# Optimization experiments

Measured on AMD Instinct MI355X. Metric: run time of the kernel, lower is better.

## Reference

```python
import jax, jax.numpy as jnp
import numpy as np

B, T, D, H = 4, 1024, 1024, 16
TP = 1024
HD = D // H
LN_EPS = 1e-3  # keras LayerNormalization default epsilon


def snac_linear(x, wt, mt):
    # conv1dsnac: w = tanh(wt) * sigmoid(mt), shape [1, nx, nf] -> [nx, nf]
    w = (jnp.tanh(wt) * jax.nn.sigmoid(mt))[0]
    return jnp.einsum('btx,xf->btf', x, w)


def layernorm(x, gamma, beta):
    mu = jnp.mean(x, axis=-1, keepdims=True)
    var = jnp.mean(jnp.square(x - mu), axis=-1, keepdims=True)
    return (x - mu) * jax.lax.rsqrt(var + LN_EPS) * gamma + beta


def setup_inputs() -> dict:
    key = jax.random.key(0)
    ks = jax.random.split(key, 10)
    s = 0.02
    return {
        'input': jax.random.normal(ks[0], (B, T, D), jnp.float32),
        'past': jax.random.normal(ks[1], (B, 2, H, TP, HD), jnp.float32),
        'qkv_wt': jax.random.normal(ks[2], (1, D, 3 * D), jnp.float32) * s,
        'qkv_mt': jax.random.normal(ks[3], (1, D, 3 * D), jnp.float32) * s,
        'merge_wt': jax.random.normal(ks[4], (1, D, D), jnp.float32) * s,
        'merge_mt': jax.random.normal(ks[5], (1, D, D), jnp.float32) * s,
        'ln1_wt': jax.random.normal(ks[6], (1, D, D), jnp.float32) * s,
        'ln1_mt': jax.random.normal(ks[7], (1, D, D), jnp.float32) * s,
        'g1': jnp.ones((D,), jnp.float32), 'b1': jnp.zeros((D,), jnp.float32),
        'g2': jnp.ones((D,), jnp.float32), 'b2': jnp.zeros((D,), jnp.float32),
    }


def reference(input, past, qkv_wt, qkv_mt, merge_wt, merge_mt, ln1_wt, ln1_mt, g1, b1, g2, b2):
    x = input
    xn = layernorm(x, g1, b1)
    c = snac_linear(xn, qkv_wt, qkv_mt)  # [B, T, 3D]
    q, k, v = jnp.split(c, 3, axis=2)
    # split heads -> [B, H, T, HD]
    to_heads = lambda t: t.reshape(B, T, H, HD).transpose(0, 2, 1, 3)
    q, k, v = to_heads(q), to_heads(k), to_heads(v)
    present = jnp.stack([k, v], axis=1)  # [B, 2, H, T, HD]
    pk, pv = past[:, 0], past[:, 1]
    k = jnp.concatenate([pk, k], axis=2)  # [B, H, TP+T, HD]
    v = jnp.concatenate([pv, v], axis=2)
    nd, ns = T, TP + T
    w = jnp.einsum('bhqd,bhkd->bhqk', q, k) * jax.lax.rsqrt(jnp.float32(HD))
    i = jnp.arange(nd)[:, None]
    j = jnp.arange(ns)[None, :]
    m = (i >= j - ns + nd).astype(w.dtype)  # [nd, ns] causal mask incl. past
    w = w * m - jnp.asarray(1e10, w.dtype) * (1 - m)
    msk = jax.nn.softmax(w, axis=-1)  # [B, H, T, TP+T]
    a = jnp.einsum('bhqk,bhkd->bhqd', msk, v)
    ah = a.transpose(0, 2, 1, 3).reshape(B, T, D)  # merge heads
    am = snac_linear(ah, merge_wt, merge_mt)
    xa = x + am
    mlp = snac_linear(layernorm(xa, g2, b2), ln1_wt, ln1_mt)
    xm = xa + mlp
    return xm, present, msk
```

## Files before the change

kernel.cpp:

```cpp
#include <hip/hip_runtime.h>
#include <hip/hip_bf16.h>

typedef _Float16 half8 __attribute__((ext_vector_type(8)));
typedef _Float16 half4v __attribute__((ext_vector_type(4)));
typedef float f32x4 __attribute__((ext_vector_type(4)));

#define DEV static __device__ __forceinline__


typedef __attribute__((address_space(1))) const unsigned int* gas_p;
typedef __attribute__((address_space(3))) unsigned int* las_p;
DEV void glds16(const void* g, void* s) {
  __builtin_amdgcn_global_load_lds((gas_p)g, (las_p)s, 16, 0, 0);
}

__global__ __launch_bounds__(256) void prep_all(const float* __restrict__ qkv_wt,
                                                const float* __restrict__ qkv_mt,
                                                const float* __restrict__ mg_wt,
                                                const float* __restrict__ mg_mt,
                                                const float* __restrict__ l1_wt,
                                                const float* __restrict__ l1_mt,
                                                _Float16* __restrict__ wq,
                                                _Float16* __restrict__ wm,
                                                _Float16* __restrict__ wl) {
  __shared__ float tile[64][65];
  const float *wt, *mt;
  _Float16* out;
  int N, bid;
  if (blockIdx.x < 768) {
    wt = qkv_wt; mt = qkv_mt; out = wq; N = 3072; bid = blockIdx.x;
  } else if (blockIdx.x < 1024) {
    wt = mg_wt; mt = mg_mt; out = wm; N = 1024; bid = blockIdx.x - 768;
  } else {
    wt = l1_wt; mt = l1_mt; out = wl; N = 1024; bid = blockIdx.x - 1024;
  }
  const int ntiles = N >> 6;
  const int nt = bid % ntiles, kt = bid / ntiles;
  const int k0 = kt << 6, n0 = nt << 6;
  const int t = threadIdx.x, r = t >> 2, c0 = (t & 3) << 4;
  const long ibase = (long)(k0 + r) * N + n0 + c0;
#pragma unroll
  for (int j = 0; j < 16; j += 4) {
    float4 a = *(const float4*)(wt + ibase + j);
    float4 b = *(const float4*)(mt + ibase + j);
    tile[r][c0 + j + 0] = tanhf(a.x) / (1.f + __expf(-b.x));
    tile[r][c0 + j + 1] = tanhf(a.y) / (1.f + __expf(-b.y));
    tile[r][c0 + j + 2] = tanhf(a.z) / (1.f + __expf(-b.z));
    tile[r][c0 + j + 3] = tanhf(a.w) / (1.f + __expf(-b.w));
  }
  __syncthreads();
  half8 o0, o1;
#pragma unroll
  for (int j = 0; j < 8; ++j) {
    o0[j] = (_Float16)tile[c0 + j][r];
    o1[j] = (_Float16)tile[c0 + 8 + j][r];
  }
  _Float16* dst = out + (long)(n0 + r) * 1024 + k0 + c0;
  *(half8*)dst = o0;
  *(half8*)(dst + 8) = o1;
}

__global__ __launch_bounds__(256) void kv_prep(const float* __restrict__ past,
                                               const _Float16* __restrict__ vnew,
                                               _Float16* __restrict__ kf,
                                               _Float16* __restrict__ vt) {
  __shared__ float tile[64][65];
  if (blockIdx.x < 4096) {
    const long e = ((long)blockIdx.x * 256 + threadIdx.x) * 4;
    const int b = (int)(e >> 20);
    const int rem = (int)(e & 1048575);
    float4 v = *(const float4*)(past + (long)b * 2097152 + rem);
    half4v o = {(_Float16)v.x, (_Float16)v.y, (_Float16)v.z, (_Float16)v.w};
    const int h = rem >> 16, td = rem & 65535;
    *(half4v*)(kf + (long)(b * 16 + h) * 131072 + td) = o;
    return;
  }
  const int bid = blockIdx.x - 4096;
  const int bh = bid >> 5, kt = bid & 31;
  const int b = bh >> 4, h = bh & 15;
  const int k0 = kt << 6;
  const int t = threadIdx.x, r = t >> 2, c0 = (t & 3) << 4;
  if (k0 < 1024) {
    const float* src = past + (((long)(b * 2 + 1) * 16 + h) * 1024 + (k0 + r)) * 64 + c0;
#pragma unroll
    for (int j = 0; j < 16; j += 4) {
      float4 v = *(const float4*)(src + j);
      tile[r][c0 + j + 0] = v.x;
      tile[r][c0 + j + 1] = v.y;
      tile[r][c0 + j + 2] = v.z;
      tile[r][c0 + j + 3] = v.w;
    }
  } else {
    const _Float16* src = vnew + ((long)bh * 1024 + (k0 - 1024 + r)) * 64 + c0;
    half8 a = *(const half8*)src;
    half8 bq = *(const half8*)(src + 8);
#pragma unroll
    for (int j = 0; j < 8; ++j) {
      tile[r][c0 + j] = (float)a[j];
      tile[r][c0 + 8 + j] = (float)bq[j];
    }
  }
  __syncthreads();
  half8 o0, o1;
#pragma unroll
  for (int j = 0; j < 8; ++j) {
    o0[j] = (_Float16)tile[c0 + j][r];
    o1[j] = (_Float16)tile[c0 + 8 + j][r];
  }
  _Float16* dst = vt + ((long)bh * 64 + r) * 2048 + k0 + c0;
  *(half8*)dst = o0;
  *(half8*)(dst + 8) = o1;
}

template <int F16IN>
__global__ __launch_bounds__(256) void ln_k(const void* __restrict__ xin,
                                            const float* __restrict__ g,
                                            const float* __restrict__ be,
                                            _Float16* __restrict__ out) {
  __shared__ float red[4];
  const int row = blockIdx.x, tid = threadIdx.x, l = tid & 63, w = tid >> 6;
  float v0, v1, v2, v3;
  if constexpr (F16IN == 0) {
    float4 v = *(const float4*)((const float*)xin + (long)row * 1024 + tid * 4);
    v0 = v.x; v1 = v.y; v2 = v.z; v3 = v.w;
  } else {
    half4v v = *(const half4v*)((const _Float16*)xin + (long)row * 1024 + tid * 4);
    v0 = (float)v[0]; v1 = (float)v[1]; v2 = (float)v[2]; v3 = (float)v[3];
  }
  float s = v0 + v1 + v2 + v3;
#pragma unroll
  for (int o = 32; o > 0; o >>= 1) s += __shfl_down(s, o, 64);
  if (l == 0) red[w] = s;
  __syncthreads();
  const float mu = (red[0] + red[1] + red[2] + red[3]) * (1.f / 1024.f);
  float dx = v0 - mu, dy = v1 - mu, dz = v2 - mu, dw = v3 - mu;
  float ss = dx * dx + dy * dy + dz * dz + dw * dw;
#pragma unroll
  for (int o = 32; o > 0; o >>= 1) ss += __shfl_down(ss, o, 64);
  __syncthreads();
  if (l == 0) red[w] = ss;
  __syncthreads();
  const float var = (red[0] + red[1] + red[2] + red[3]) * (1.f / 1024.f);
  const float rs = rsqrtf(var + 1e-3f);
  float4 gv = *(const float4*)(g + tid * 4);
  float4 bv = *(const float4*)(be + tid * 4);
  half4v o = {(_Float16)(dx * rs * gv.x + bv.x), (_Float16)(dy * rs * gv.y + bv.y),
              (_Float16)(dz * rs * gv.z + bv.z), (_Float16)(dw * rs * gv.w + bv.w)};
  *(half4v*)(out + (long)row * 1024 + tid * 4) = o;
}

template <int BM, int EPI>
__global__ __launch_bounds__(256) void gemm_k(const _Float16* __restrict__ A,
                                              const _Float16* __restrict__ Bt,
                                              int mtiles,
                                              _Float16* __restrict__ e_q,
                                              _Float16* __restrict__ e_k,
                                              _Float16* __restrict__ e_v,
                                              float* __restrict__ e_present,
                                              const void* __restrict__ e_resv,
                                              void* __restrict__ e_outv) {
  constexpr int FM = BM / 32;
  __shared__ __align__(16) char smem[2 * BM * 128 + 32768];
  char* Bbase = smem + 2 * BM * 128;
  const int tid = threadIdx.x, l = tid & 63, w = tid >> 6;
  const int wm = w >> 1, wn = w & 1;
  const int bm = blockIdx.x % mtiles, bn = blockIdx.x / mtiles;
  const long m0 = (long)bm * BM, n0 = (long)bn * 128;

  f32x4 acc[FM][4];
#pragma unroll
  for (int i = 0; i < FM; ++i)
#pragma unroll
    for (int j = 0; j < 4; ++j) acc[i][j] = (f32x4){0.f, 0.f, 0.f, 0.f};

  auto stage = [&](int b, int kt) {
#pragma unroll
    for (int i = 0; i < FM; ++i) {
      const int cid = i * 256 + tid, row = cid >> 3, u = cid & 7;
      glds16(A + (m0 + row) * 1024 + kt * 64 + ((u ^ (row & 7)) << 3),
             smem + b * BM * 128 + i * 4096 + w * 1024);
    }
#pragma unroll
    for (int i = 0; i < 4; ++i) {
      const int cid = i * 256 + tid, row = cid >> 3, u = cid & 7;
      glds16(Bt + (n0 + row) * 1024 + kt * 64 + ((u ^ (row & 7)) << 3),
             Bbase + b * 16384 + i * 4096 + w * 1024);
    }
  };

  stage(0, 0);
  __syncthreads();
  for (int kt = 0; kt < 16; ++kt) {
    const int cur = kt & 1;
    if (kt < 15) stage(cur ^ 1, kt + 1);
    const char* As = smem + cur * BM * 128;
    const char* Bs = Bbase + cur * 16384;
    __builtin_amdgcn_s_setprio(1);
#pragma unroll
    for (int k2 = 0; k2 < 2; ++k2) {
      const int sl = k2 * 4 + (l >> 4);
      half8 bfr[4];
#pragma unroll
      for (int fn = 0; fn < 4; ++fn) {
        const int rn = wn * 64 + fn * 16 + (l & 15);
        bfr[fn] = *(const half8*)(Bs + rn * 128 + ((sl ^ (rn & 7)) << 4));
      }
#pragma unroll
      for (int fm = 0; fm < FM; ++fm) {
        const int rm = wm * (BM / 2) + fm * 16 + (l & 15);
        const half8 afr = *(const half8*)(As + rm * 128 + ((sl ^ (rm & 7)) << 4));
#pragma unroll
        for (int fn = 0; fn < 4; ++fn)
          acc[fm][fn] = __builtin_amdgcn_mfma_f32_16x16x32_f16(afr, bfr[fn], acc[fm][fn], 0, 0, 0);
      }
    }
    __builtin_amdgcn_s_setprio(0);
    __syncthreads();
  }
#pragma unroll
  for (int fm = 0; fm < FM; ++fm) {
#pragma unroll
    for (int fn = 0; fn < 4; ++fn) {
#pragma unroll
      for (int r = 0; r < 4; ++r) {
        const long row = m0 + wm * (BM / 2) + fm * 16 + (l >> 4) * 4 + r;
        const long col = n0 + fn * 16 + (l & 15) + wn * 64;
        const float v = acc[fm][fn][r];
        if constexpr (EPI == 0) {
          const int b = (int)(row >> 10), t = (int)(row & 1023);
          const int sec = (int)(col >> 10), h = ((int)col >> 6) & 15, hd = (int)col & 63;
          const long bh = b * 16 + h;
          if (sec == 0) {
            e_q[(bh * 1024 + t) * 64 + hd] = (_Float16)v;
          } else if (sec == 1) {
            e_present[(((long)(b * 2) * 16 + h) * 1024 + t) * 64 + hd] = v;
            e_k[(bh * 2048 + 1024 + t) * 64 + hd] = (_Float16)v;
          } else {
            e_present[(((long)(b * 2 + 1) * 16 + h) * 1024 + t) * 64 + hd] = v;
            e_v[(bh * 1024 + t) * 64 + hd] = (_Float16)v;
          }
        } else if constexpr (EPI == 1) {
          ((_Float16*)e_outv)[row * 1024 + col] =
              (_Float16)(((const float*)e_resv)[row * 1024 + col] + v);
        } else {
          ((float*)e_outv)[row * 1024 + col] =
              (float)((const _Float16*)e_resv)[row * 1024 + col] + v;
        }
      }
    }
  }
}

__global__ __launch_bounds__(256, 4) void attn_k(const _Float16* __restrict__ qg,
                                                 const _Float16* __restrict__ kg,
                                                 const _Float16* __restrict__ vtg,
                                                 float* __restrict__ msk,
                                                 _Float16* __restrict__ ah) {
  __shared__ __align__(16) char smem[40960];
  char* ps_all = smem + 32768;
  const int tid = threadIdx.x, l = tid & 63, w = tid >> 6;
  char* psw = ps_all + w * 2048;
  const int lq = l & 15, hi = l >> 4;

  const int x = blockIdx.x & 7, g = blockIdx.x >> 3;
  const int bh = (g & 7) * 8 + x;
  const int qt = 15 - (g >> 3);
  const int r0 = qt << 6;
  const int rowg0 = r0 + w * 16;

  const _Float16* kb = kg + (long)bh * 131072;
  const _Float16* vb = vtg + (long)bh * 131072;
  float* mskb = msk + ((long)bh * 1024 + rowg0) * 2048;

  half8 qa[2];
  {
    const _Float16* qp = qg + ((long)bh * 1024 + rowg0 + lq) * 64 + hi * 8;
    qa[0] = *(const half8*)qp;
    qa[1] = *(const half8*)(qp + 32);
  }

  constexpr float C1 = 0.125f * 1.44269504088896341f;
  const int lim = rowg0 + lq + 1024;

  const int nc1 = (r0 + 1215) >> 7;
  auto stageK128 = [&](int b, int c) {
#pragma unroll
    for (int i = 0; i < 4; ++i) {
      const int cid = i * 256 + tid, row = cid >> 3, u = cid & 7;
      glds16(kb + (long)(c * 128 + row) * 64 + ((u ^ (row & 7)) << 3),
             smem + b * 16384 + i * 4096 + w * 1024);
    }
  };
  float rsum = 0.f;
  stageK128(0, 0);
  __syncthreads();
  for (int c = 0; c < nc1; ++c) {
    const int cur = c & 1;
    if (c + 1 < nc1) stageK128(cur ^ 1, c + 1);
    const char* ks = smem + cur * 16384;
    f32x4 sa[8];
#pragma unroll
    for (int fn = 0; fn < 8; ++fn) sa[fn] = (f32x4){0.f, 0.f, 0.f, 0.f};
    __builtin_amdgcn_s_setprio(1);
#pragma unroll
    for (int k2 = 0; k2 < 2; ++k2) {
      const int sl = k2 * 4 + hi;
      half8 ak[8];
#pragma unroll
      for (int fn = 0; fn < 8; ++fn) {
        const int rn = fn * 16 + lq;
        ak[fn] = *(const half8*)(ks + rn * 128 + ((sl ^ (rn & 7)) << 4));
      }
#pragma unroll
      for (int fn = 0; fn < 8; ++fn)
        sa[fn] = __builtin_amdgcn_mfma_f32_16x16x32_f16(ak[fn], qa[k2], sa[fn], 0, 0, 0);
    }
    __builtin_amdgcn_s_setprio(0);
    if (c < nc1 - 1) {
#pragma unroll
      for (int fn = 0; fn < 8; ++fn)
#pragma unroll
        for (int r = 0; r < 4; ++r) rsum += __builtin_amdgcn_exp2f(sa[fn][r] * C1);
    } else {
#pragma unroll
      for (int fn = 0; fn < 8; ++fn)
#pragma unroll
        for (int r = 0; r < 4; ++r) {
          const int col = c * 128 + fn * 16 + hi * 4 + r;
          const float e = __builtin_amdgcn_exp2f(sa[fn][r] * C1);
          rsum += (col <= lim) ? e : 0.f;
        }
    }
    __syncthreads();
  }
  rsum += __shfl_xor(rsum, 16, 64);
  rsum += __shfl_xor(rsum, 32, 64);
  const float c2s = -__builtin_amdgcn_logf(rsum);

  const int nc = (r0 + 1151) >> 6;
  auto stageK = [&](int b, int c) {
#pragma unroll
    for (int i = 0; i < 2; ++i) {
      const int cid = i * 256 + tid, row = cid >> 3, u = cid & 7;
      glds16(kb + (long)(c * 64 + row) * 64 + ((u ^ (row & 7)) << 3),
             smem + b * 8192 + i * 4096 + w * 1024);
    }
  };
  auto stageV = [&](int b, int c) {
#pragma unroll
    for (int i = 0; i < 2; ++i) {
      const int cid = i * 256 + tid, row = cid >> 3, u = cid & 7;
      glds16(vb + (long)row * 2048 + c * 64 + ((u ^ (row & 7)) << 3),
             smem + 16384 + b * 8192 + i * 4096 + w * 1024);
    }
  };

  f32x4 pv[4];
#pragma unroll
  for (int j = 0; j < 4; ++j) pv[j] = (f32x4){0.f, 0.f, 0.f, 0.f};
  __syncthreads();
  stageK(0, 0);
  stageV(0, 0);
  __syncthreads();
  for (int c = 0; c < nc; ++c) {
    const int cur = c & 1;
    if (c + 1 < nc) {
      stageK(cur ^ 1, c + 1);
      stageV(cur ^ 1, c + 1);
    }
    const char* ks = smem + cur * 8192;
    f32x4 sa[4];
#pragma unroll
    for (int fn = 0; fn < 4; ++fn) sa[fn] = (f32x4){0.f, 0.f, 0.f, 0.f};
    __builtin_amdgcn_s_setprio(1);
#pragma unroll
    for (int k2 = 0; k2 < 2; ++k2) {
      const int sl = k2 * 4 + hi;
      half8 ak[4];
#pragma unroll
      for (int fn = 0; fn < 4; ++fn) {
        const int rn = fn * 16 + lq;
        ak[fn] = *(const half8*)(ks + rn * 128 + ((sl ^ (rn & 7)) << 4));
      }
#pragma unroll
      for (int fn = 0; fn < 4; ++fn)
        sa[fn] = __builtin_amdgcn_mfma_f32_16x16x32_f16(ak[fn], qa[k2], sa[fn], 0, 0, 0);
    }
    __builtin_amdgcn_s_setprio(0);
    const bool bound = (c == nc - 1);
#pragma unroll
    for (int fn = 0; fn < 4; ++fn) {
      float pr[4];
#pragma unroll
      for (int r = 0; r < 4; ++r) {
        float p = __builtin_amdgcn_exp2f(sa[fn][r] * C1 + c2s);
        if (bound) {
          const int col = c * 64 + fn * 16 + hi * 4 + r;
          p = (col <= lim) ? p : 0.f;
        }
        pr[r] = p;
      }
      *(float4*)(mskb + (long)lq * 2048 + c * 64 + fn * 16 + hi * 4) =
          make_float4(pr[0], pr[1], pr[2], pr[3]);
      const half4v hv = {(_Float16)pr[0], (_Float16)pr[1], (_Float16)pr[2],
                         (_Float16)pr[3]};
      const int bc = fn * 32 + hi * 8;
      *(half4v*)(psw + lq * 128 + ((((bc >> 4) ^ (lq & 7)) << 4) | (bc & 15))) = hv;
    }
    __builtin_amdgcn_wave_barrier();
    asm volatile("s_waitcnt lgkmcnt(0)" ::: "memory");
    __builtin_amdgcn_sched_barrier(0);
    const char* vs = smem + 16384 + cur * 8192;
    __builtin_amdgcn_s_setprio(1);
#pragma unroll
    for (int k2p = 0; k2p < 2; ++k2p) {
      const int sl2 = k2p * 4 + hi;
      const half8 pa = *(const half8*)(psw + lq * 128 + ((sl2 ^ (lq & 7)) << 4));
      half8 bv[4];
#pragma unroll
      for (int fn2 = 0; fn2 < 4; ++fn2) {
        const int rd = fn2 * 16 + lq;
        bv[fn2] = *(const half8*)(vs + rd * 128 + ((sl2 ^ (rd & 7)) << 4));
      }
#pragma unroll
      for (int fn2 = 0; fn2 < 4; ++fn2)
        pv[fn2] = __builtin_amdgcn_mfma_f32_16x16x32_f16(pa, bv[fn2], pv[fn2], 0, 0, 0);
    }
    __builtin_amdgcn_s_setprio(0);
    __syncthreads();
  }

  const int ntail = 512 - (nc << 4);
  if (ntail > 0) {
    const float4 z4 = make_float4(0.f, 0.f, 0.f, 0.f);
    for (int row = 0; row < 16; ++row)
      for (int i = l; i < ntail; i += 64)
        *(float4*)(mskb + (long)row * 2048 + nc * 64 + i * 4) = z4;
  }

  const int b_ = bh >> 4, h_ = bh & 15;
  _Float16* ahb = ah + ((long)b_ * 1024 + rowg0) * 1024 + h_ * 64;
#pragma unroll
  for (int fn2 = 0; fn2 < 4; ++fn2)
#pragma unroll
    for (int r = 0; r < 4; ++r)
      ahb[(long)(hi * 4 + r) * 1024 + fn2 * 16 + lq] = (_Float16)pv[fn2][r];
}

extern "C" void kernel_launch(void* const* d_in, const int* in_sizes, int n_in,
                              void* d_out, int out_size, void* d_ws, size_t ws_size,
                              hipStream_t stream) {
  const float* x = (const float*)d_in[0];
  const float* past = (const float*)d_in[1];
  const float* qkv_wt = (const float*)d_in[2];
  const float* qkv_mt = (const float*)d_in[3];
  const float* merge_wt = (const float*)d_in[4];
  const float* merge_mt = (const float*)d_in[5];
  const float* ln1_wt = (const float*)d_in[6];
  const float* ln1_mt = (const float*)d_in[7];
  const float* g1 = (const float*)d_in[8];
  const float* b1 = (const float*)d_in[9];
  const float* g2 = (const float*)d_in[10];
  const float* b2 = (const float*)d_in[11];

  float* out = (float*)d_out;
  float* o_xm = out;
  float* o_present = out + 4194304;
  float* o_msk = out + 4194304 + 8388608;

  char* ws = (char*)d_ws;
  _Float16* wq_t = (_Float16*)(ws + 0);
  _Float16* wm_t = (_Float16*)(ws + 6291456);
  _Float16* wl_t = (_Float16*)(ws + 8388608);
  _Float16* xn   = (_Float16*)(ws + 10485760);
  _Float16* qws  = (_Float16*)(ws + 18874368);
  _Float16* kful = (_Float16*)(ws + 27262976);
  _Float16* vnew = (_Float16*)(ws + 44040192);
  _Float16* vt   = (_Float16*)(ws + 52428800);
  _Float16* ah   = (_Float16*)(ws + 69206016);
  _Float16* xa   = (_Float16*)(ws + 77594624);

  prep_all<<<1280, 256, 0, stream>>>(qkv_wt, qkv_mt, merge_wt, merge_mt, ln1_wt,
                                     ln1_mt, wq_t, wm_t, wl_t);
  ln_k<0><<<4096, 256, 0, stream>>>(x, g1, b1, xn);
  gemm_k<128, 0><<<768, 256, 0, stream>>>(xn, wq_t, 32, qws, kful, vnew, o_present,
                                          nullptr, nullptr);
  kv_prep<<<6144, 256, 0, stream>>>(past, vnew, kful, vt);
  attn_k<<<1024, 256, 0, stream>>>(qws, kful, vt, o_msk, ah);
  gemm_k<64, 1><<<512, 256, 0, stream>>>(ah, wm_t, 64, nullptr, nullptr, nullptr,
                                         nullptr, x, xa);
  ln_k<1><<<4096, 256, 0, stream>>>(xa, g2, b2, xn);
  gemm_k<64, 2><<<512, 256, 0, stream>>>(xn, wl_t, 64, nullptr, nullptr, nullptr,
                                         nullptr, xa, o_xm);
}
```

Baseline: 289.0 us.

## Drop GEMM LDS double buffering and use 64x64 tiles for merge/MLP GEMMs

The GEMM kernel now stages A and B into a single LDS buffer each k-step and waits on a barrier before computing, instead of prefetching the next k-tile into a second buffer. It also gains a BN template parameter so the merge and MLP projections can run 64x64 tiles over 1024 blocks instead of 64x128 over 512. The aim is to cut LDS use per block so more blocks fit per CU, and to spread the small GEMMs across more workgroups. The cost is that global-to-LDS loads no longer overlap MFMA work within a block, so the kernel must rely on other resident blocks to hide load latency. Each block also reuses less data with the smaller tiles.

```diff
diff --git a/kernel.cpp b/kernel.cpp
--- a/kernel.cpp
+++ b/kernel.cpp
@@ -149,7 +149,7 @@
   *(half4v*)(out + (long)row * 1024 + tid * 4) = o;
 }
 
-template <int BM, int EPI>
+template <int BM, int BN, int EPI>
 __global__ __launch_bounds__(256) void gemm_k(const _Float16* __restrict__ A,
                                               const _Float16* __restrict__ Bt,
                                               int mtiles,
@@ -159,50 +159,43 @@
                                               float* __restrict__ e_present,
                                               const void* __restrict__ e_resv,
                                               void* __restrict__ e_outv) {
-  constexpr int FM = BM / 32;
-  __shared__ __align__(16) char smem[2 * BM * 128 + 32768];
-  char* Bbase = smem + 2 * BM * 128;
+  constexpr int FM = BM / 32, FN = BN / 32;
+  __shared__ __align__(16) char smem[BM * 128 + BN * 128];
+  char* As = smem;
+  char* Bs = smem + BM * 128;
   const int tid = threadIdx.x, l = tid & 63, w = tid >> 6;
   const int wm = w >> 1, wn = w & 1;
   const int bm = blockIdx.x % mtiles, bn = blockIdx.x / mtiles;
-  const long m0 = (long)bm * BM, n0 = (long)bn * 128;
-
-  f32x4 acc[FM][4];
+  const long m0 = (long)bm * BM, n0 = (long)bn * BN;
+
+  f32x4 acc[FM][FN];
 #pragma unroll
   for (int i = 0; i < FM; ++i)
 #pragma unroll
-    for (int j = 0; j < 4; ++j) acc[i][j] = (f32x4){0.f, 0.f, 0.f, 0.f};
-
-  auto stage = [&](int b, int kt) {
+    for (int j = 0; j < FN; ++j) acc[i][j] = (f32x4){0.f, 0.f, 0.f, 0.f};
+
+  for (int kt = 0; kt < 16; ++kt) {
 #pragma unroll
     for (int i = 0; i < FM; ++i) {
       const int cid = i * 256 + tid, row = cid >> 3, u = cid & 7;
       glds16(A + (m0 + row) * 1024 + kt * 64 + ((u ^ (row & 7)) << 3),
-             smem + b * BM * 128 + i * 4096 + w * 1024);
-    }
-#pragma unroll
-    for (int i = 0; i < 4; ++i) {
+             As + i * 4096 + w * 1024);
+    }
+#pragma unroll
+    for (int i = 0; i < FN; ++i) {
       const int cid = i * 256 + tid, row = cid >> 3, u = cid & 7;
       glds16(Bt + (n0 + row) * 1024 + kt * 64 + ((u ^ (row & 7)) << 3),
-             Bbase + b * 16384 + i * 4096 + w * 1024);
-    }
-  };
-
-  stage(0, 0);
-  __syncthreads();
-  for (int kt = 0; kt < 16; ++kt) {
-    const int cur = kt & 1;
-    if (kt < 15) stage(cur ^ 1, kt + 1);
-    const char* As = smem + cur * BM * 128;
-    const char* Bs = Bbase + cur * 16384;
+             Bs + i * 4096 + w * 1024);
+    }
+    __syncthreads();
     __builtin_amdgcn_s_setprio(1);
 #pragma unroll
     for (int k2 = 0; k2 < 2; ++k2) {
       const int sl = k2 * 4 + (l >> 4);
-      half8 bfr[4];
-#pragma unroll
-      for (int fn = 0; fn < 4; ++fn) {
-        const int rn = wn * 64 + fn * 16 + (l & 15);
+      half8 bfr[FN];
+#pragma unroll
+      for (int fn = 0; fn < FN; ++fn) {
+        const int rn = wn * (BN / 2) + fn * 16 + (l & 15);
         bfr[fn] = *(const half8*)(Bs + rn * 128 + ((sl ^ (rn & 7)) << 4));
       }
 #pragma unroll
@@ -210,7 +203,7 @@
         const int rm = wm * (BM / 2) + fm * 16 + (l & 15);
         const half8 afr = *(const half8*)(As + rm * 128 + ((sl ^ (rm & 7)) << 4));
 #pragma unroll
-        for (int fn = 0; fn < 4; ++fn)
+        for (int fn = 0; fn < FN; ++fn)
           acc[fm][fn] = __builtin_amdgcn_mfma_f32_16x16x32_f16(afr, bfr[fn], acc[fm][fn], 0, 0, 0);
       }
     }
@@ -220,11 +213,11 @@
 #pragma unroll
   for (int fm = 0; fm < FM; ++fm) {
 #pragma unroll
-    for (int fn = 0; fn < 4; ++fn) {
+    for (int fn = 0; fn < FN; ++fn) {
 #pragma unroll
       for (int r = 0; r < 4; ++r) {
         const long row = m0 + wm * (BM / 2) + fm * 16 + (l >> 4) * 4 + r;
-        const long col = n0 + fn * 16 + (l & 15) + wn * 64;
+        const long col = n0 + wn * (BN / 2) + fn * 16 + (l & 15);
         const float v = acc[fm][fn][r];
         if constexpr (EPI == 0) {
           const int b = (int)(row >> 10), t = (int)(row & 1023);
@@ -483,13 +476,13 @@
   prep_all<<<1280, 256, 0, stream>>>(qkv_wt, qkv_mt, merge_wt, merge_mt, ln1_wt,
                                      ln1_mt, wq_t, wm_t, wl_t);
   ln_k<0><<<4096, 256, 0, stream>>>(x, g1, b1, xn);
-  gemm_k<128, 0><<<768, 256, 0, stream>>>(xn, wq_t, 32, qws, kful, vnew, o_present,
-                                          nullptr, nullptr);
+  gemm_k<128, 128, 0><<<768, 256, 0, stream>>>(xn, wq_t, 32, qws, kful, vnew,
+                                               o_present, nullptr, nullptr);
   kv_prep<<<6144, 256, 0, stream>>>(past, vnew, kful, vt);
   attn_k<<<1024, 256, 0, stream>>>(qws, kful, vt, o_msk, ah);
-  gemm_k<64, 1><<<512, 256, 0, stream>>>(ah, wm_t, 64, nullptr, nullptr, nullptr,
-                                         nullptr, x, xa);
+  gemm_k<64, 64, 1><<<1024, 256, 0, stream>>>(ah, wm_t, 64, nullptr, nullptr,
+                                              nullptr, nullptr, x, xa);
   ln_k<1><<<4096, 256, 0, stream>>>(xa, g2, b2, xn);
-  gemm_k<64, 2><<<512, 256, 0, stream>>>(xn, wl_t, 64, nullptr, nullptr, nullptr,
-                                         nullptr, xa, o_xm);
-}
+  gemm_k<64, 64, 2><<<1024, 256, 0, stream>>>(xn, wl_t, 64, nullptr, nullptr,
+                                              nullptr, nullptr, xa, o_xm);
+}
```

Result: slower. 315.6 us (+9.2%).
